# Optimization experiments

Measured on AMD Instinct MI355X. Metric: run time of the kernel, lower is better.

Reference implementation:

```python
import jax, jax.numpy as jnp
import numpy as np

N_CELLS = 1024
IN_DIM = 256
HID = 512
OUT_DIM = 256
INNER = 128
N_PAIRS = N_CELLS // 2
N_FACTIONS = 8
SYNC = 0.15
DEBATE = 0.15


def setup_inputs() -> dict:
    key = jax.random.key(0)
    ks = jax.random.split(key, 20)
    s = 0.05
    d = {
        "x": jax.random.normal(ks[0], (1, IN_DIM), jnp.float32),
        "hiddens": jax.random.normal(ks[1], (N_CELLS, HID), jnp.float32) * 0.1,
        "W1a": jax.random.normal(ks[2], (INNER, IN_DIM + HID), jnp.float32) * s,
        "b1a": jax.random.normal(ks[3], (INNER,), jnp.float32) * s,
        "W2a": jax.random.normal(ks[4], (OUT_DIM, INNER), jnp.float32) * s,
        "b2a": jax.random.normal(ks[5], (OUT_DIM,), jnp.float32) * s,
        "W1g": jax.random.normal(ks[6], (INNER, IN_DIM + HID), jnp.float32) * s,
        "b1g": jax.random.normal(ks[7], (INNER,), jnp.float32) * s,
        "W2g": jax.random.normal(ks[8], (OUT_DIM, INNER), jnp.float32) * s,
        "b2g": jax.random.normal(ks[9], (OUT_DIM,), jnp.float32) * s,
        "w_ih": jax.random.normal(ks[10], (3 * HID, OUT_DIM + 1), jnp.float32) * s,
        "w_hh": jax.random.normal(ks[11], (3 * HID, HID), jnp.float32) * s,
        "b_ih": jax.random.normal(ks[12], (3 * HID,), jnp.float32) * s,
        "b_hh": jax.random.normal(ks[13], (3 * HID,), jnp.float32) * s,
        "head_w": jax.random.normal(ks[14], (IN_DIM, OUT_DIM), jnp.float32) * s,
        "head_b": jax.random.normal(ks[15], (IN_DIM,), jnp.float32) * s,
        "entanglement": jnp.ones((N_PAIRS,), jnp.float32) * 0.5,
        "bell_rotations": jax.random.normal(ks[16], (N_PAIRS, HID, HID), jnp.float32) * 0.01,
        "step": 8,
    }
    return d


def _mlp(c, W1, b1, W2, b2):
    return jax.nn.relu(c @ W1.T + b1) @ W2.T + b2


def _gru(mem, h, w_ih, w_hh, b_ih, b_hh):
    gi = mem @ w_ih.T + b_ih  # [N, 3H]
    gh = h @ w_hh.T + b_hh
    i_r, i_z, i_n = jnp.split(gi, 3, axis=-1)
    h_r, h_z, h_n = jnp.split(gh, 3, axis=-1)
    r = jax.nn.sigmoid(i_r + h_r)
    z = jax.nn.sigmoid(i_z + h_z)
    n = jnp.tanh(i_n + r * h_n)
    return (1.0 - z) * n + z * h


def reference(x, hiddens, W1a, b1a, W2a, b2a, W1g, b1g, W2g, b2g,
              w_ih, w_hh, b_ih, b_hh, head_w, head_b,
              entanglement, bell_rotations, step):
    sg = jax.lax.stop_gradient
    # --- per-cell MLP (vectorized over cells) ---
    xb = jnp.broadcast_to(x, (N_CELLS, IN_DIM))
    combined = jnp.concatenate([xb, hiddens], axis=-1)  # [N, IN+HID]
    a = _mlp(combined, W1a, b1a, W2a, b2a)
    g = _mlp(combined, W1g, b1g, W2g, b2g)
    output = a - g                                  # [N, OUT]
    tension = jnp.mean(output ** 2, axis=-1)        # [N]
    mem_input = sg(jnp.concatenate([output, tension[:, None]], axis=-1))
    new_h = _gru(mem_input, hiddens, w_ih, w_hh, b_ih, b_hh)
    h = sg(new_h)  # hiddens are detached buffers in torch
    # --- bell correlations (rotation via .data, e via .item -> no grads) ---
    hp = h.reshape(N_PAIRS, 2, HID)
    h_i, h_j = hp[:, 0], hp[:, 1]
    e = sg(jax.nn.sigmoid(entanglement))[:, None]   # [P,1]
    rot = jnp.tanh(sg(bell_rotations))              # [P,H,H]
    mixed_i = (1.0 - e) * h_i + e * jnp.einsum('pab,pb->pa', rot, h_j)
    mixed_j = (1.0 - e) * h_j + e * jnp.einsum('pba,pb->pa', rot, h_i)
    h = jnp.stack([mixed_i, -mixed_j], axis=1).reshape(N_CELLS, HID)
    # --- faction sync / debate ---
    fs = N_CELLS // N_FACTIONS
    hr = h.reshape(N_FACTIONS, fs, HID)
    fmean = hr.mean(axis=1, keepdims=True)
    hr = (1.0 - SYNC) * hr + SYNC * fmean
    if step > 5:
        global_opinion = hr.mean(axis=1).mean(axis=0)  # mean of post-sync faction means
        dc = max(1, fs // 4)
        hr = hr.at[:, :dc].set((1.0 - DEBATE) * hr[:, :dc] + DEBATE * global_opinion)
    h = hr.reshape(N_CELLS, HID)
    # --- tension-weighted output combine ---
    weights = jax.nn.softmax(sg(tension))           # detached in torch
    combined_out = (weights[None, :] @ output)      # [1, OUT]
    pred = combined_out @ head_w.T + head_b         # [1, IN]
    avg_tension = tension.mean()
    return pred, avg_tension, h
```

## Files before the change

### kernel.cpp

```cpp
#include <hip/hip_runtime.h>
#include <math.h>

#define NCELLS 1024
#define INDIM 256
#define HID 512
#define ODIM 256
#define NPAIRS 512

typedef __attribute__((ext_vector_type(4))) float f32x4;
typedef __attribute__((ext_vector_type(8))) short short8;
typedef unsigned short ushort_t;

__device__ inline float sigm(float x){ return 1.0f/(1.0f + expf(-x)); }
__device__ inline float tanh3(float x){ return x*fmaf(x*x, -0.33333334f, 1.0f); }
__device__ inline ushort_t f2bf(float f){
    unsigned u = __float_as_uint(f);
    return (ushort_t)((u + 0x7FFFu + ((u>>16)&1u)) >> 16);
}

__global__ __launch_bounds__(64) void k_cvt(
    const float* __restrict__ x, const float* __restrict__ hiddens,
    const float* __restrict__ W1a, const float* __restrict__ W1g,
    const float* __restrict__ W2a, const float* __restrict__ W2g,
    const float* __restrict__ w_ih, const float* __restrict__ w_hh,
    const float* __restrict__ b1a, const float* __restrict__ b1g,
    const float* __restrict__ b2a, const float* __restrict__ b2g,
    ushort_t* __restrict__ Wc1f, ushort_t* __restrict__ Wc2f,
    ushort_t* __restrict__ wihf, ushort_t* __restrict__ whhf,
    ushort_t* __restrict__ combf, ushort_t* __restrict__ hiddf,
    float* __restrict__ bc1, float* __restrict__ bc2, float* __restrict__ wcol)
{
    const int b = blockIdx.x;
    const int lane = threadIdx.x;
    if (b >= 5376){
        int t = (b - 5376)*64 + lane;
        if (t < 256)       bc1[t] = (t<128) ? b1a[t] : b1g[t-128];
        else if (t < 512)  { int i=t-256; bc2[i] = b2a[i] - b2g[i]; }
        else               { int i=t-512; wcol[i] = w_ih[(size_t)i*257 + 256]; }
        return;
    }
    int job, idx, KT; ushort_t* dst;
    if      (b < 384){  job=0; idx=b;      KT=24; dst=Wc1f; }
    else if (b < 512){  job=1; idx=b-384;  KT=8;  dst=Wc2f; }
    else if (b < 1280){ job=2; idx=b-512;  KT=8;  dst=wihf; }
    else if (b < 2816){ job=3; idx=b-1280; KT=16; dst=whhf; }
    else if (b < 4352){ job=4; idx=b-2816; KT=24; dst=combf;}
    else             {  job=5; idx=b-4352; KT=16; dst=hiddf;}
    const int rt = idx / KT, kt = idx % KT;
    const int r  = rt*16 + (lane & 15);
    const int kb = kt*32 + (lane >> 4)*8;
    float v[8];
    if (job == 0){
        const float* s = (r < 128) ? (W1a + (size_t)r*768) : (W1g + (size_t)(r-128)*768);
        #pragma unroll
        for (int j=0;j<8;++j) v[j] = s[kb+j];
    } else if (job == 1){
        if (kb < 128){ const float* s = W2a + (size_t)r*128 + kb;
            #pragma unroll
            for (int j=0;j<8;++j) v[j] = s[j];
        } else { const float* s = W2g + (size_t)r*128 + (kb-128);
            #pragma unroll
            for (int j=0;j<8;++j) v[j] = -s[j];
        }
    } else if (job == 2){
        const float* s = w_ih + (size_t)r*257 + kb;
        #pragma unroll
        for (int j=0;j<8;++j) v[j] = s[j];
    } else if (job == 3){
        const float* s = w_hh + (size_t)r*512 + kb;
        #pragma unroll
        for (int j=0;j<8;++j) v[j] = s[j];
    } else if (job == 4){
        if (kb < 256){
            #pragma unroll
            for (int j=0;j<8;++j) v[j] = x[kb+j];
        } else { const float* s = hiddens + (size_t)r*512 + (kb-256);
            #pragma unroll
            for (int j=0;j<8;++j) v[j] = s[j];
        }
    } else {
        const float* s = hiddens + (size_t)r*512 + kb;
        #pragma unroll
        for (int j=0;j<8;++j) v[j] = s[j];
    }
    short8 o;
    #pragma unroll
    for (int j=0;j<8;++j) o[j] = (short)f2bf(v[j]);
    ((short8*)dst)[(size_t)idx*64 + lane] = o;
}

template<int KT, int EPI>
__global__ __launch_bounds__(256) void k_mm(
    const ushort_t* __restrict__ Af, const ushort_t* __restrict__ Bf,
    const float* __restrict__ bias, float* __restrict__ C,
    ushort_t* __restrict__ Cf, int N)
{
    const int lane = threadIdx.x & 63;
    const int w    = threadIdx.x >> 6;
    const int mtile = blockIdx.y*4 + w;
    const int nt0   = blockIdx.x*2;
    const short8* A8 = (const short8*)Af;
    const short8* B8 = (const short8*)Bf;
    f32x4 acc0 = {0.f,0.f,0.f,0.f}, acc1 = {0.f,0.f,0.f,0.f};
    #pragma unroll 4
    for (int kt=0; kt<KT; ++kt){
        short8 a  = A8[((size_t)mtile*KT + kt)*64 + lane];
        short8 b0 = B8[((size_t)nt0*KT + kt)*64 + lane];
        short8 b1 = B8[((size_t)(nt0+1)*KT + kt)*64 + lane];
        acc0 = __builtin_amdgcn_mfma_f32_16x16x32_bf16(a, b0, acc0, 0,0,0);
        acc1 = __builtin_amdgcn_mfma_f32_16x16x32_bf16(a, b1, acc1, 0,0,0);
    }
    if (EPI == 0){
        const int r0 = mtile*16 + (lane>>4)*4;
        const int c0 = nt0*16 + (lane&15);
        const float bb0 = bias[c0], bb1 = bias[c0+16];
        #pragma unroll
        for (int i=0;i<4;++i){
            C[(size_t)(r0+i)*N + c0]    = acc0[i] + bb0;
            C[(size_t)(r0+i)*N + c0+16] = acc1[i] + bb1;
        }
    } else {
        __shared__ float lt[4][16][33];
        const int rr = (lane>>4)*4, cc = lane&15;
        const float bb0 = bias[nt0*16 + cc], bb1 = bias[nt0*16 + 16 + cc];
        #pragma unroll
        for (int i=0;i<4;++i){
            lt[w][rr+i][cc]    = fmaxf(acc0[i] + bb0, 0.f);
            lt[w][rr+i][16+cc] = fmaxf(acc1[i] + bb1, 0.f);
        }
        __syncthreads();
        const int m = lane & 15, kb = (lane>>4)*8;
        short8 o;
        #pragma unroll
        for (int j=0;j<8;++j) o[j] = (short)f2bf(lt[w][m][kb+j]);
        ((short8*)Cf)[((size_t)mtile*gridDim.x + blockIdx.x)*64 + lane] = o;
    }
}

__global__ __launch_bounds__(512) void k_tension_cvt(const float* __restrict__ OUT,
        float* __restrict__ tension, ushort_t* __restrict__ Of)
{
    const int mt = blockIdx.x;
    const int lane = threadIdx.x & 63, wv = threadIdx.x >> 6;
    const int m = mt*16 + (lane&15);
    const int k = wv*32 + (lane>>4)*8;
    const float* p = OUT + (size_t)m*ODIM + k;
    float4 v0 = *(const float4*)p;
    float4 v1 = *(const float4*)(p+4);
    float s = v0.x*v0.x + v0.y*v0.y + v0.z*v0.z + v0.w*v0.w
            + v1.x*v1.x + v1.y*v1.y + v1.z*v1.z + v1.w*v1.w;
    short8 o;
    o[0]=(short)f2bf(v0.x); o[1]=(short)f2bf(v0.y); o[2]=(short)f2bf(v0.z); o[3]=(short)f2bf(v0.w);
    o[4]=(short)f2bf(v1.x); o[5]=(short)f2bf(v1.y); o[6]=(short)f2bf(v1.z); o[7]=(short)f2bf(v1.w);
    ((short8*)Of)[((size_t)mt*8 + wv)*64 + lane] = o;
    s += __shfl_xor(s, 16); s += __shfl_xor(s, 32);
    __shared__ float red[8][16];
    if (lane < 16) red[wv][lane] = s;
    __syncthreads();
    if (threadIdx.x < 16){
        float t = 0.f;
        #pragma unroll
        for (int q=0;q<8;++q) t += red[q][threadIdx.x];
        tension[mt*16 + threadIdx.x] = t * (1.0f/ODIM);
    }
}

__global__ __launch_bounds__(512) void k_mix(const float* __restrict__ GI,
        const float* __restrict__ GH, const float* __restrict__ tension,
        const float* __restrict__ wcol, const float* __restrict__ hiddens,
        const float* __restrict__ bell, const float* __restrict__ ent,
        float* __restrict__ hmix)
{
    const int p = blockIdx.x;
    const int tid = threadIdx.x;
    const int lane = tid & 63;
    const int wv = tid >> 6;
    __shared__ __align__(16) float hi[HID], hj[HID];
    __shared__ __align__(16) float colacc[8][HID];
    {
        const int j = tid;
        const float wj0 = wcol[j], wj1 = wcol[512+j], wj2 = wcol[1024+j];
        #pragma unroll
        for (int c01=0; c01<2; ++c01){
            const int cell = 2*p + c01;
            const float tv = tension[cell];
            const float* gi = GI + (size_t)cell*1536;
            const float* gh = GH + (size_t)cell*1536;
            float rg = sigm(gi[j]      + tv*wj0 + gh[j]);
            float zg = sigm(gi[512+j]  + tv*wj1 + gh[512+j]);
            float nn = tanhf(gi[1024+j]+ tv*wj2 + rg*gh[1024+j]);
            float h  = (1.f - zg)*nn + zg*hiddens[(size_t)cell*HID + j];
            (c01 ? hj : hi)[j] = h;
        }
    }
    __syncthreads();
    const float* __restrict__ rot = bell + (size_t)p * HID * HID;
    const float e = 1.0f/(1.0f + expf(-ent[p]));
    const float one_e = 1.0f - e;
    const int c0 = lane<<2, c1 = 256 + (lane<<2);
    float hjr[8];
    #pragma unroll
    for (int k=0;k<4;++k){ hjr[k]=hj[c0+k]; hjr[4+k]=hj[c1+k]; }
    float aj[8] = {};
    #pragma unroll 2
    for (int r = wv; r < HID; r += 8) {
        float4 v0 = *(const float4*)(rot + (size_t)r*HID + c0);
        float4 v1 = *(const float4*)(rot + (size_t)r*HID + c1);
        float t[8];
        t[0]=tanh3(v0.x); t[1]=tanh3(v0.y); t[2]=tanh3(v0.z); t[3]=tanh3(v0.w);
        t[4]=tanh3(v1.x); t[5]=tanh3(v1.y); t[6]=tanh3(v1.z); t[7]=tanh3(v1.w);
        const float hir = hi[r];
        float rp = 0.0f;
        #pragma unroll
        for (int k=0;k<8;++k){ rp = fmaf(t[k], hjr[k], rp); aj[k] = fmaf(t[k], hir, aj[k]); }
        #pragma unroll
        for (int m=1;m<64;m<<=1) rp += __shfl_xor(rp, m);
        if (lane == 0) hmix[(size_t)(2*p)*HID + r] = one_e*hir + e*rp;
    }
    *(float4*)&colacc[wv][c0] = make_float4(aj[0],aj[1],aj[2],aj[3]);
    *(float4*)&colacc[wv][c1] = make_float4(aj[4],aj[5],aj[6],aj[7]);
    __syncthreads();
    float s = 0.0f;
    #pragma unroll
    for (int w=0;w<8;++w) s += colacc[w][tid];
    hmix[(size_t)(2*p+1)*HID + tid] = -(one_e*hj[tid] + e*s);
}

__global__ __launch_bounds__(512) void k_fmean(const float* __restrict__ hmix, float* __restrict__ fmean){
    int f = blockIdx.x, d = threadIdx.x;
    float s = 0.0f;
    for (int c=0;c<128;++c) s += hmix[(size_t)((f<<7)+c)*HID + d];
    fmean[f*HID + d] = s*(1.0f/128.0f);
}

__global__ __launch_bounds__(512) void k_final_h(const float* __restrict__ hmix,
        const float* __restrict__ fmean, const int* __restrict__ stepp, float* __restrict__ hout){
    int cell = blockIdx.x, d = threadIdx.x;
    int f = cell >> 7;
    float v = 0.85f*hmix[(size_t)cell*HID + d] + 0.15f*fmean[f*HID + d];
    if (*stepp > 5 && (cell & 127) < 32){
        float g = 0.0f;
        #pragma unroll
        for (int q=0;q<8;++q) g += fmean[q*HID + d];
        g *= 0.125f;
        v = 0.85f*v + 0.15f*g;
    }
    hout[(size_t)cell*HID + d] = v;
}

__global__ __launch_bounds__(1024) void k_softmax(const float* __restrict__ tension,
        float* __restrict__ weights, float* __restrict__ avg_out){
    int t = threadIdx.x;
    int lane = t & 63, wv = t >> 6;
    float tv = tension[t];
    __shared__ float red[16], redb[16], SS[2];
    float m = tv;
    #pragma unroll
    for (int s=1;s<64;s<<=1) m = fmaxf(m, __shfl_xor(m, s));
    if (lane==0) red[wv] = m;
    __syncthreads();
    if (t==0){ float mm=red[0]; for(int i=1;i<16;++i) mm=fmaxf(mm,red[i]); SS[1]=mm; }
    __syncthreads();
    float M = SS[1];
    float ex = expf(tv - M);
    float s2 = ex, s3 = tv;
    #pragma unroll
    for (int s=1;s<64;s<<=1){ s2 += __shfl_xor(s2,s); s3 += __shfl_xor(s3,s); }
    if (lane==0){ red[wv]=s2; redb[wv]=s3; }
    __syncthreads();
    if (t==0){
        float a=0,b=0;
        for(int i=0;i<16;++i){ a+=red[i]; b+=redb[i]; }
        SS[0]=a;
        avg_out[0] = b*(1.0f/1024.0f);
    }
    __syncthreads();
    weights[t] = ex / SS[0];
}

__global__ __launch_bounds__(256) void k_copart(const float* __restrict__ OUT,
        const float* __restrict__ weights, float* __restrict__ copart){
    int b = blockIdx.x, c = threadIdx.x;
    float s = 0.0f;
    for (int r = b*32; r < b*32+32; ++r) s = fmaf(weights[r], OUT[(size_t)r*ODIM + c], s);
    copart[b*ODIM + c] = s;
}

__global__ __launch_bounds__(256) void k_pred(const float* __restrict__ copart,
        const float* __restrict__ head_w, const float* __restrict__ head_b, float* __restrict__ pred){
    int o = threadIdx.x;
    __shared__ float co[ODIM];
    float s = 0.0f;
    for (int b=0;b<32;++b) s += copart[b*ODIM + o];
    co[o] = s;
    __syncthreads();
    float acc = head_b[o];
    for (int c=0;c<ODIM;++c) acc = fmaf(head_w[(size_t)o*ODIM + c], co[c], acc);
    pred[o] = acc;
}

extern "C" void kernel_launch(void* const* d_in, const int* in_sizes, int n_in,
                              void* d_out, int out_size, void* d_ws, size_t ws_size,
                              hipStream_t stream)
{
    const float* x      = (const float*)d_in[0];
    const float* hiddens= (const float*)d_in[1];
    const float* W1a=(const float*)d_in[2];  const float* b1a=(const float*)d_in[3];
    const float* W2a=(const float*)d_in[4];  const float* b2a=(const float*)d_in[5];
    const float* W1g=(const float*)d_in[6];  const float* b1g=(const float*)d_in[7];
    const float* W2g=(const float*)d_in[8];  const float* b2g=(const float*)d_in[9];
    const float* w_ih=(const float*)d_in[10]; const float* w_hh=(const float*)d_in[11];
    const float* b_ih=(const float*)d_in[12]; const float* b_hh=(const float*)d_in[13];
    const float* head_w=(const float*)d_in[14]; const float* head_b=(const float*)d_in[15];
    const float* ent=(const float*)d_in[16]; const float* bell=(const float*)d_in[17];
    const int*   stepp=(const int*)d_in[18];
    float* out = (float*)d_out;

    char* wsb = (char*)d_ws;
    size_t off = 0;
    auto carve = [&](size_t bytes)->char*{ char* p = wsb + off; off += (bytes + 63) & ~(size_t)63; return p; };
    ushort_t* combf = (ushort_t*)carve((size_t)1024*768*2);
    ushort_t* hiddf = (ushort_t*)carve((size_t)1024*512*2);
    ushort_t* Wc1f  = (ushort_t*)carve((size_t)256*768*2);
    ushort_t* Wc2f  = (ushort_t*)carve((size_t)256*256*2);
    ushort_t* wihf  = (ushort_t*)carve((size_t)1536*256*2);
    ushort_t* whhf  = (ushort_t*)carve((size_t)1536*512*2);
    ushort_t* H1f   = (ushort_t*)carve((size_t)1024*256*2);
    ushort_t* Of    = (ushort_t*)carve((size_t)1024*256*2);
    float* bc1   = (float*)carve(256*4);
    float* bc2   = (float*)carve(256*4);
    float* wcol  = (float*)carve(1536*4);
    float* OUT   = (float*)carve((size_t)1024*256*4);
    float* tension=(float*)carve(1024*4);
    float* GI    = (float*)carve((size_t)1024*1536*4);
    float* GH    = (float*)carve((size_t)1024*1536*4);
    float* hmix  = (float*)carve((size_t)1024*512*4);
    float* fmean = (float*)carve(8*512*4);
    float* weights=(float*)carve(1024*4);
    float* copart =(float*)carve(32*256*4);

    k_cvt<<<5408, 64, 0, stream>>>(x, hiddens, W1a, W1g, W2a, W2g, w_ih, w_hh,
                                   b1a, b1g, b2a, b2g,
                                   Wc1f, Wc2f, wihf, whhf, combf, hiddf, bc1, bc2, wcol);
    k_mm<24,1><<<dim3(8,16), 256, 0, stream>>>(combf, Wc1f, bc1, nullptr, H1f, 256);
    k_mm<8,0><<<dim3(8,16), 256, 0, stream>>>(H1f, Wc2f, bc2, OUT, nullptr, 256);
    k_tension_cvt<<<64, 512, 0, stream>>>(OUT, tension, Of);
    k_mm<16,0><<<dim3(48,16), 256, 0, stream>>>(hiddf, whhf, b_hh, GH, nullptr, 1536);
    k_mm<8,0><<<dim3(48,16), 256, 0, stream>>>(Of, wihf, b_ih, GI, nullptr, 1536);
    k_mix<<<512, 512, 0, stream>>>(GI, GH, tension, wcol, hiddens, bell, ent, hmix);
    k_fmean<<<8, 512, 0, stream>>>(hmix, fmean);
    k_final_h<<<1024, 512, 0, stream>>>(hmix, fmean, stepp, out + 257);
    k_softmax<<<1, 1024, 0, stream>>>(tension, weights, out + 256);
    k_copart<<<32, 256, 0, stream>>>(OUT, weights, copart);
    k_pred<<<1, 256, 0, stream>>>(copart, head_w, head_b, out);
}
```

Before: 164.1 us.

## Fuse MLP, tension and GRU gate GEMMs into one per-row-tile kernel

Replaces the activation-conversion pass and four separate GEMM launches plus the tension kernel with a single k_fwd kernel. Each block owns 16 cells, converts x/hiddens to bf16 in LDS, chains both MLP layers, computes tension, and runs the GRU input and hidden GEMMs from LDS. The r/z gate sums from the two GEMMs are accumulated together into one GS buffer, cutting the intermediate writes. The cost is only 64 blocks of 256 threads doing all of the GEMM work, which leaves most CUs idle and may limit throughput.

```diff
diff --git a/kernel.cpp b/kernel.cpp
--- a/kernel.cpp
+++ b/kernel.cpp
@@ -2,7 +2,6 @@
 #include <math.h>
 
 #define NCELLS 1024
-#define INDIM 256
 #define HID 512
 #define ODIM 256
 #define NPAIRS 512
@@ -17,9 +16,14 @@
     unsigned u = __float_as_uint(f);
     return (ushort_t)((u + 0x7FFFu + ((u>>16)&1u)) >> 16);
 }
-
-__global__ __launch_bounds__(64) void k_cvt(
-    const float* __restrict__ x, const float* __restrict__ hiddens,
+__device__ inline short8 pack8(float4 v0, float4 v1){
+    short8 o;
+    o[0]=(short)f2bf(v0.x); o[1]=(short)f2bf(v0.y); o[2]=(short)f2bf(v0.z); o[3]=(short)f2bf(v0.w);
+    o[4]=(short)f2bf(v1.x); o[5]=(short)f2bf(v1.y); o[6]=(short)f2bf(v1.z); o[7]=(short)f2bf(v1.w);
+    return o;
+}
+
+__global__ __launch_bounds__(256) void k_cvtw(
     const float* __restrict__ W1a, const float* __restrict__ W1g,
     const float* __restrict__ W2a, const float* __restrict__ W2g,
     const float* __restrict__ w_ih, const float* __restrict__ w_hh,
@@ -27,33 +31,34 @@
     const float* __restrict__ b2a, const float* __restrict__ b2g,
     ushort_t* __restrict__ Wc1f, ushort_t* __restrict__ Wc2f,
     ushort_t* __restrict__ wihf, ushort_t* __restrict__ whhf,
-    ushort_t* __restrict__ combf, ushort_t* __restrict__ hiddf,
     float* __restrict__ bc1, float* __restrict__ bc2, float* __restrict__ wcol)
 {
-    const int b = blockIdx.x;
-    const int lane = threadIdx.x;
-    if (b >= 5376){
-        int t = (b - 5376)*64 + lane;
-        if (t < 256)       bc1[t] = (t<128) ? b1a[t] : b1g[t-128];
-        else if (t < 512)  { int i=t-256; bc2[i] = b2a[i] - b2g[i]; }
-        else               { int i=t-512; wcol[i] = w_ih[(size_t)i*257 + 256]; }
+    const int t = threadIdx.x;
+    if (blockIdx.x == 704){
+        #pragma unroll
+        for (int i=0;i<8;++i){
+            int id = i*256 + t;
+            if (id < 256)      bc1[id] = (id<128) ? b1a[id] : b1g[id-128];
+            else if (id < 512){ int k=id-256; bc2[k] = b2a[k] - b2g[k]; }
+            else              { int k=id-512; wcol[k] = w_ih[(size_t)k*257 + 256]; }
+        }
         return;
     }
+    const int T = blockIdx.x*4 + (t>>6);
+    const int lane = t & 63;
     int job, idx, KT; ushort_t* dst;
-    if      (b < 384){  job=0; idx=b;      KT=24; dst=Wc1f; }
-    else if (b < 512){  job=1; idx=b-384;  KT=8;  dst=Wc2f; }
-    else if (b < 1280){ job=2; idx=b-512;  KT=8;  dst=wihf; }
-    else if (b < 2816){ job=3; idx=b-1280; KT=16; dst=whhf; }
-    else if (b < 4352){ job=4; idx=b-2816; KT=24; dst=combf;}
-    else             {  job=5; idx=b-4352; KT=16; dst=hiddf;}
+    if      (T < 384){  job=0; idx=T;      KT=24; dst=Wc1f; }
+    else if (T < 512){  job=1; idx=T-384;  KT=8;  dst=Wc2f; }
+    else if (T < 1280){ job=2; idx=T-512;  KT=8;  dst=wihf; }
+    else             {  job=3; idx=T-1280; KT=16; dst=whhf; }
     const int rt = idx / KT, kt = idx % KT;
     const int r  = rt*16 + (lane & 15);
     const int kb = kt*32 + (lane >> 4)*8;
     float v[8];
     if (job == 0){
-        const float* s = (r < 128) ? (W1a + (size_t)r*768) : (W1g + (size_t)(r-128)*768);
-        #pragma unroll
-        for (int j=0;j<8;++j) v[j] = s[kb+j];
+        const float* s = (r < 128) ? (W1a + (size_t)r*768 + kb) : (W1g + (size_t)(r-128)*768 + kb);
+        #pragma unroll
+        for (int j=0;j<8;++j) v[j] = s[j];
     } else if (job == 1){
         if (kb < 128){ const float* s = W2a + (size_t)r*128 + kb;
             #pragma unroll
@@ -66,20 +71,8 @@
         const float* s = w_ih + (size_t)r*257 + kb;
         #pragma unroll
         for (int j=0;j<8;++j) v[j] = s[j];
-    } else if (job == 3){
+    } else {
         const float* s = w_hh + (size_t)r*512 + kb;
-        #pragma unroll
-        for (int j=0;j<8;++j) v[j] = s[j];
-    } else if (job == 4){
-        if (kb < 256){
-            #pragma unroll
-            for (int j=0;j<8;++j) v[j] = x[kb+j];
-        } else { const float* s = hiddens + (size_t)r*512 + (kb-256);
-            #pragma unroll
-            for (int j=0;j<8;++j) v[j] = s[j];
-        }
-    } else {
-        const float* s = hiddens + (size_t)r*512 + kb;
         #pragma unroll
         for (int j=0;j<8;++j) v[j] = s[j];
     }
@@ -89,85 +82,184 @@
     ((short8*)dst)[(size_t)idx*64 + lane] = o;
 }
 
-template<int KT, int EPI>
-__global__ __launch_bounds__(256) void k_mm(
-    const ushort_t* __restrict__ Af, const ushort_t* __restrict__ Bf,
-    const float* __restrict__ bias, float* __restrict__ C,
-    ushort_t* __restrict__ Cf, int N)
+__global__ __launch_bounds__(256) void k_fwd(
+    const float* __restrict__ x, const float* __restrict__ hiddens,
+    const ushort_t* __restrict__ Wc1f, const ushort_t* __restrict__ Wc2f,
+    const ushort_t* __restrict__ wihf, const ushort_t* __restrict__ whhf,
+    const float* __restrict__ bc1, const float* __restrict__ bc2,
+    const float* __restrict__ b_ih, const float* __restrict__ b_hh,
+    float* __restrict__ OUT, float* __restrict__ tension,
+    float* __restrict__ GS, float* __restrict__ GIn, float* __restrict__ GHn)
 {
-    const int lane = threadIdx.x & 63;
-    const int w    = threadIdx.x >> 6;
-    const int mtile = blockIdx.y*4 + w;
-    const int nt0   = blockIdx.x*2;
-    const short8* A8 = (const short8*)Af;
-    const short8* B8 = (const short8*)Bf;
-    f32x4 acc0 = {0.f,0.f,0.f,0.f}, acc1 = {0.f,0.f,0.f,0.f};
-    #pragma unroll 4
-    for (int kt=0; kt<KT; ++kt){
-        short8 a  = A8[((size_t)mtile*KT + kt)*64 + lane];
-        short8 b0 = B8[((size_t)nt0*KT + kt)*64 + lane];
-        short8 b1 = B8[((size_t)(nt0+1)*KT + kt)*64 + lane];
-        acc0 = __builtin_amdgcn_mfma_f32_16x16x32_bf16(a, b0, acc0, 0,0,0);
-        acc1 = __builtin_amdgcn_mfma_f32_16x16x32_bf16(a, b1, acc1, 0,0,0);
-    }
-    if (EPI == 0){
-        const int r0 = mtile*16 + (lane>>4)*4;
-        const int c0 = nt0*16 + (lane&15);
-        const float bb0 = bias[c0], bb1 = bias[c0+16];
-        #pragma unroll
-        for (int i=0;i<4;++i){
-            C[(size_t)(r0+i)*N + c0]    = acc0[i] + bb0;
-            C[(size_t)(r0+i)*N + c0+16] = acc1[i] + bb1;
-        }
-    } else {
-        __shared__ float lt[4][16][33];
-        const int rr = (lane>>4)*4, cc = lane&15;
-        const float bb0 = bias[nt0*16 + cc], bb1 = bias[nt0*16 + 16 + cc];
-        #pragma unroll
-        for (int i=0;i<4;++i){
-            lt[w][rr+i][cc]    = fmaxf(acc0[i] + bb0, 0.f);
-            lt[w][rr+i][16+cc] = fmaxf(acc1[i] + bb1, 0.f);
-        }
-        __syncthreads();
-        const int m = lane & 15, kb = (lane>>4)*8;
-        short8 o;
-        #pragma unroll
-        for (int j=0;j<8;++j) o[j] = (short)f2bf(lt[w][m][kb+j]);
-        ((short8*)Cf)[((size_t)mtile*gridDim.x + blockIdx.x)*64 + lane] = o;
-    }
-}
-
-__global__ __launch_bounds__(512) void k_tension_cvt(const float* __restrict__ OUT,
-        float* __restrict__ tension, ushort_t* __restrict__ Of)
-{
-    const int mt = blockIdx.x;
-    const int lane = threadIdx.x & 63, wv = threadIdx.x >> 6;
-    const int m = mt*16 + (lane&15);
-    const int k = wv*32 + (lane>>4)*8;
-    const float* p = OUT + (size_t)m*ODIM + k;
-    float4 v0 = *(const float4*)p;
-    float4 v1 = *(const float4*)(p+4);
-    float s = v0.x*v0.x + v0.y*v0.y + v0.z*v0.z + v0.w*v0.w
-            + v1.x*v1.x + v1.y*v1.y + v1.z*v1.z + v1.w*v1.w;
-    short8 o;
-    o[0]=(short)f2bf(v0.x); o[1]=(short)f2bf(v0.y); o[2]=(short)f2bf(v0.z); o[3]=(short)f2bf(v0.w);
-    o[4]=(short)f2bf(v1.x); o[5]=(short)f2bf(v1.y); o[6]=(short)f2bf(v1.z); o[7]=(short)f2bf(v1.w);
-    ((short8*)Of)[((size_t)mt*8 + wv)*64 + lane] = o;
-    s += __shfl_xor(s, 16); s += __shfl_xor(s, 32);
-    __shared__ float red[8][16];
-    if (lane < 16) red[wv][lane] = s;
-    __syncthreads();
-    if (threadIdx.x < 16){
-        float t = 0.f;
-        #pragma unroll
-        for (int q=0;q<8;++q) t += red[q][threadIdx.x];
-        tension[mt*16 + threadIdx.x] = t * (1.0f/ODIM);
-    }
-}
-
-__global__ __launch_bounds__(512) void k_mix(const float* __restrict__ GI,
-        const float* __restrict__ GH, const float* __restrict__ tension,
-        const float* __restrict__ wcol, const float* __restrict__ hiddens,
+    const int r0 = blockIdx.x*16;
+    const int t = threadIdx.x;
+    const int lane = t & 63, w = t >> 6;
+    __shared__ short8 lds_comb[24*64];
+    __shared__ short8 lds_h1[8*64];
+    __shared__ short8 lds_of[8*64];
+    __shared__ __align__(16) float lds_tile[16][264];
+    const short8* B1 = (const short8*)Wc1f;
+    const short8* B2 = (const short8*)Wc2f;
+    const short8* Bi = (const short8*)wihf;
+    const short8* Bh = (const short8*)whhf;
+
+    #pragma unroll
+    for (int s6=0; s6<6; ++s6){
+        int s = t + s6*256;
+        int kt = s>>6, ln = s&63;
+        int row = r0 + (ln&15);
+        int cb = kt*32 + ((ln>>4)<<3);
+        const float* src = (cb < 256) ? (x + cb) : (hiddens + (size_t)row*HID + (cb-256));
+        float4 v0 = *(const float4*)src;
+        float4 v1 = *(const float4*)(src+4);
+        lds_comb[s] = pack8(v0, v1);
+    }
+    __syncthreads();
+
+    {
+        f32x4 acc[4] = {{0,0,0,0},{0,0,0,0},{0,0,0,0},{0,0,0,0}};
+        for (int kt=0; kt<24; ++kt){
+            short8 a = lds_comb[kt*64 + lane];
+            #pragma unroll
+            for (int c=0;c<4;++c){
+                short8 b = B1[((w*4+c)*24 + kt)*64 + lane];
+                acc[c] = __builtin_amdgcn_mfma_f32_16x16x32_bf16(a, b, acc[c], 0,0,0);
+            }
+        }
+        const int rb = (lane>>4)*4;
+        #pragma unroll
+        for (int c=0;c<4;++c){
+            int col = w*64 + c*16 + (lane&15);
+            float bb = bc1[col];
+            #pragma unroll
+            for (int i=0;i<4;++i)
+                lds_tile[rb+i][col] = fmaxf(acc[c][i] + bb, 0.f);
+        }
+    }
+    __syncthreads();
+    #pragma unroll
+    for (int s2=0; s2<2; ++s2){
+        int s = t + s2*256;
+        int ln = s&63;
+        int row = ln&15, cb = (s>>6)*32 + ((ln>>4)<<3);
+        float4 v0 = *(const float4*)&lds_tile[row][cb];
+        float4 v1 = *(const float4*)&lds_tile[row][cb+4];
+        lds_h1[s] = pack8(v0, v1);
+    }
+    __syncthreads();
+    {
+        f32x4 acc[4] = {{0,0,0,0},{0,0,0,0},{0,0,0,0},{0,0,0,0}};
+        for (int kt=0; kt<8; ++kt){
+            short8 a = lds_h1[kt*64 + lane];
+            #pragma unroll
+            for (int c=0;c<4;++c){
+                short8 b = B2[((w*4+c)*8 + kt)*64 + lane];
+                acc[c] = __builtin_amdgcn_mfma_f32_16x16x32_bf16(a, b, acc[c], 0,0,0);
+            }
+        }
+        const int rb = (lane>>4)*4;
+        #pragma unroll
+        for (int c=0;c<4;++c){
+            int col = w*64 + c*16 + (lane&15);
+            float bb = bc2[col];
+            #pragma unroll
+            for (int i=0;i<4;++i)
+                lds_tile[rb+i][col] = acc[c][i] + bb;
+        }
+    }
+    __syncthreads();
+    {
+        int row = t>>4, seg = t&15;
+        float s = 0.f;
+        #pragma unroll
+        for (int c=0;c<16;++c){ float v = lds_tile[row][seg*16+c]; s = fmaf(v,v,s); }
+        s += __shfl_xor(s,1); s += __shfl_xor(s,2); s += __shfl_xor(s,4); s += __shfl_xor(s,8);
+        if (seg == 0) tension[r0+row] = s * (1.0f/ODIM);
+    }
+    #pragma unroll
+    for (int s4=0; s4<4; ++s4){
+        int s = t + s4*256;
+        int row = s>>6, c4 = s&63;
+        float4 v = *(const float4*)&lds_tile[row][c4*4];
+        *(float4*)&OUT[(size_t)(r0+row)*ODIM + c4*4] = v;
+    }
+    #pragma unroll
+    for (int s2=0; s2<2; ++s2){
+        int s = t + s2*256;
+        int ln = s&63;
+        int row = ln&15, cb = (s>>6)*32 + ((ln>>4)<<3);
+        float4 v0 = *(const float4*)&lds_tile[row][cb];
+        float4 v1 = *(const float4*)&lds_tile[row][cb+4];
+        lds_of[s] = pack8(v0, v1);
+    }
+    __syncthreads();
+    const int rb = (lane>>4)*4;
+    for (int c6=0; c6<6; ++c6){
+        const int g = w + 4*c6;
+        const int nt0 = g*4;
+        if (nt0 < 64){
+            f32x4 acc[4] = {{0,0,0,0},{0,0,0,0},{0,0,0,0},{0,0,0,0}};
+            for (int kt=0; kt<8; ++kt){
+                short8 a = lds_of[kt*64 + lane];
+                #pragma unroll
+                for (int c=0;c<4;++c){
+                    short8 b = Bi[((nt0+c)*8 + kt)*64 + lane];
+                    acc[c] = __builtin_amdgcn_mfma_f32_16x16x32_bf16(a, b, acc[c], 0,0,0);
+                }
+            }
+            for (int kt=0; kt<16; ++kt){
+                short8 a = lds_comb[(8+kt)*64 + lane];
+                #pragma unroll
+                for (int c=0;c<4;++c){
+                    short8 b = Bh[((nt0+c)*16 + kt)*64 + lane];
+                    acc[c] = __builtin_amdgcn_mfma_f32_16x16x32_bf16(a, b, acc[c], 0,0,0);
+                }
+            }
+            #pragma unroll
+            for (int c=0;c<4;++c){
+                int n = (nt0+c)*16 + (lane&15);
+                float bb = b_ih[n] + b_hh[n];
+                #pragma unroll
+                for (int i=0;i<4;++i)
+                    GS[(size_t)(r0+rb+i)*1024 + n] = acc[c][i] + bb;
+            }
+        } else {
+            f32x4 ai[4] = {{0,0,0,0},{0,0,0,0},{0,0,0,0},{0,0,0,0}};
+            f32x4 ah[4] = {{0,0,0,0},{0,0,0,0},{0,0,0,0},{0,0,0,0}};
+            for (int kt=0; kt<8; ++kt){
+                short8 a = lds_of[kt*64 + lane];
+                #pragma unroll
+                for (int c=0;c<4;++c){
+                    short8 b = Bi[((nt0+c)*8 + kt)*64 + lane];
+                    ai[c] = __builtin_amdgcn_mfma_f32_16x16x32_bf16(a, b, ai[c], 0,0,0);
+                }
+            }
+            for (int kt=0; kt<16; ++kt){
+                short8 a = lds_comb[(8+kt)*64 + lane];
+                #pragma unroll
+                for (int c=0;c<4;++c){
+                    short8 b = Bh[((nt0+c)*16 + kt)*64 + lane];
+                    ah[c] = __builtin_amdgcn_mfma_f32_16x16x32_bf16(a, b, ah[c], 0,0,0);
+                }
+            }
+            #pragma unroll
+            for (int c=0;c<4;++c){
+                int j = (nt0+c-64)*16 + (lane&15);
+                float bi = b_ih[1024+j], bh = b_hh[1024+j];
+                #pragma unroll
+                for (int i=0;i<4;++i){
+                    GIn[(size_t)(r0+rb+i)*HID + j] = ai[c][i] + bi;
+                    GHn[(size_t)(r0+rb+i)*HID + j] = ah[c][i] + bh;
+                }
+            }
+        }
+    }
+}
+
+__global__ __launch_bounds__(512) void k_mix(const float* __restrict__ GS,
+        const float* __restrict__ GIn, const float* __restrict__ GHn,
+        const float* __restrict__ tension, const float* __restrict__ wcol,
+        const float* __restrict__ hiddens,
         const float* __restrict__ bell, const float* __restrict__ ent,
         float* __restrict__ hmix)
 {
@@ -184,11 +276,10 @@
         for (int c01=0; c01<2; ++c01){
             const int cell = 2*p + c01;
             const float tv = tension[cell];
-            const float* gi = GI + (size_t)cell*1536;
-            const float* gh = GH + (size_t)cell*1536;
-            float rg = sigm(gi[j]      + tv*wj0 + gh[j]);
-            float zg = sigm(gi[512+j]  + tv*wj1 + gh[512+j]);
-            float nn = tanhf(gi[1024+j]+ tv*wj2 + rg*gh[1024+j]);
+            const float* gs = GS + (size_t)cell*1024;
+            float rg = sigm(gs[j]     + tv*wj0);
+            float zg = sigm(gs[512+j] + tv*wj1);
+            float nn = tanhf(GIn[(size_t)cell*HID + j] + tv*wj2 + rg*GHn[(size_t)cell*HID + j]);
             float h  = (1.f - zg)*nn + zg*hiddens[(size_t)cell*HID + j];
             (c01 ? hj : hi)[j] = h;
         }
@@ -206,13 +297,13 @@
     for (int r = wv; r < HID; r += 8) {
         float4 v0 = *(const float4*)(rot + (size_t)r*HID + c0);
         float4 v1 = *(const float4*)(rot + (size_t)r*HID + c1);
-        float t[8];
-        t[0]=tanh3(v0.x); t[1]=tanh3(v0.y); t[2]=tanh3(v0.z); t[3]=tanh3(v0.w);
-        t[4]=tanh3(v1.x); t[5]=tanh3(v1.y); t[6]=tanh3(v1.z); t[7]=tanh3(v1.w);
+        float tt[8];
+        tt[0]=tanh3(v0.x); tt[1]=tanh3(v0.y); tt[2]=tanh3(v0.z); tt[3]=tanh3(v0.w);
+        tt[4]=tanh3(v1.x); tt[5]=tanh3(v1.y); tt[6]=tanh3(v1.z); tt[7]=tanh3(v1.w);
         const float hir = hi[r];
         float rp = 0.0f;
         #pragma unroll
-        for (int k=0;k<8;++k){ rp = fmaf(t[k], hjr[k], rp); aj[k] = fmaf(t[k], hir, aj[k]); }
+        for (int k=0;k<8;++k){ rp = fmaf(tt[k], hjr[k], rp); aj[k] = fmaf(tt[k], hir, aj[k]); }
         #pragma unroll
         for (int m=1;m<64;m<<=1) rp += __shfl_xor(rp, m);
         if (lane == 0) hmix[(size_t)(2*p)*HID + r] = one_e*hir + e*rp;
@@ -319,35 +410,30 @@
     char* wsb = (char*)d_ws;
     size_t off = 0;
     auto carve = [&](size_t bytes)->char*{ char* p = wsb + off; off += (bytes + 63) & ~(size_t)63; return p; };
-    ushort_t* combf = (ushort_t*)carve((size_t)1024*768*2);
-    ushort_t* hiddf = (ushort_t*)carve((size_t)1024*512*2);
     ushort_t* Wc1f  = (ushort_t*)carve((size_t)256*768*2);
     ushort_t* Wc2f  = (ushort_t*)carve((size_t)256*256*2);
     ushort_t* wihf  = (ushort_t*)carve((size_t)1536*256*2);
     ushort_t* whhf  = (ushort_t*)carve((size_t)1536*512*2);
-    ushort_t* H1f   = (ushort_t*)carve((size_t)1024*256*2);
-    ushort_t* Of    = (ushort_t*)carve((size_t)1024*256*2);
     float* bc1   = (float*)carve(256*4);
     float* bc2   = (float*)carve(256*4);
     float* wcol  = (float*)carve(1536*4);
     float* OUT   = (float*)carve((size_t)1024*256*4);
     float* tension=(float*)carve(1024*4);
-    float* GI    = (float*)carve((size_t)1024*1536*4);
-    float* GH    = (float*)carve((size_t)1024*1536*4);
+    float* GS    = (float*)carve((size_t)1024*1024*4);
+    float* GIn   = (float*)carve((size_t)1024*512*4);
+    float* GHn   = (float*)carve((size_t)1024*512*4);
     float* hmix  = (float*)carve((size_t)1024*512*4);
     float* fmean = (float*)carve(8*512*4);
     float* weights=(float*)carve(1024*4);
     float* copart =(float*)carve(32*256*4);
 
-    k_cvt<<<5408, 64, 0, stream>>>(x, hiddens, W1a, W1g, W2a, W2g, w_ih, w_hh,
-                                   b1a, b1g, b2a, b2g,
-                                   Wc1f, Wc2f, wihf, whhf, combf, hiddf, bc1, bc2, wcol);
-    k_mm<24,1><<<dim3(8,16), 256, 0, stream>>>(combf, Wc1f, bc1, nullptr, H1f, 256);
-    k_mm<8,0><<<dim3(8,16), 256, 0, stream>>>(H1f, Wc2f, bc2, OUT, nullptr, 256);
-    k_tension_cvt<<<64, 512, 0, stream>>>(OUT, tension, Of);
-    k_mm<16,0><<<dim3(48,16), 256, 0, stream>>>(hiddf, whhf, b_hh, GH, nullptr, 1536);
-    k_mm<8,0><<<dim3(48,16), 256, 0, stream>>>(Of, wihf, b_ih, GI, nullptr, 1536);
-    k_mix<<<512, 512, 0, stream>>>(GI, GH, tension, wcol, hiddens, bell, ent, hmix);
+    k_cvtw<<<705, 256, 0, stream>>>(W1a, W1g, W2a, W2g, w_ih, w_hh,
+                                    b1a, b1g, b2a, b2g,
+                                    Wc1f, Wc2f, wihf, whhf, bc1, bc2, wcol);
+    k_fwd<<<64, 256, 0, stream>>>(x, hiddens, Wc1f, Wc2f, wihf, whhf,
+                                  bc1, bc2, b_ih, b_hh,
+                                  OUT, tension, GS, GIn, GHn);
+    k_mix<<<512, 512, 0, stream>>>(GS, GIn, GHn, tension, wcol, hiddens, bell, ent, hmix);
     k_fmean<<<8, 512, 0, stream>>>(hmix, fmean);
     k_final_h<<<1024, 512, 0, stream>>>(hmix, fmean, stepp, out + 257);
     k_softmax<<<1, 1024, 0, stream>>>(tension, weights, out + 256);
```

Measured after the change: 169.9 us. 3.5% more time.
